# Kernel optimization log

Hardware: AMD Instinct MI355X
Metric: run time of the kernel (lower is better)

## Reference

```python
import jax, jax.numpy as jnp
import numpy as np

C = 128                      # channels per irrep
LS = [0, 0, 1, 1, 2, 2]      # active irreps (0e,0o,1e,1o,2e,2o), sorted order
D = C * sum(2 * l + 1 for l in LS)  # 2304
N = 100000                   # nodes


def setup_inputs() -> dict:
    key = jax.random.key(0)
    ks = jax.random.split(key, 7)
    inp = {"x": jax.random.normal(ks[0], (N, D), dtype=jnp.float32)}
    scale = 1.0 / np.sqrt(C)
    for name, k in zip(["W0p", "W0m", "W1p", "W1m", "W2p", "W2m"], ks[1:]):
        inp[name] = jax.random.normal(k, (C, C), dtype=jnp.float32) * scale
    return inp


def reference(x, W0p, W0m, W1p, W1m, W2p, W2m):
    # Split flat features into per-(l,parity) blocks [N, C, 2l+1],
    # mix channels per irrep (movedim + Linear in torch == einsum here),
    # merge back and add residual.
    Ws = [W0p, W0m, W1p, W1m, W2p, W2m]
    idx = 0
    parts = []
    for l, W in zip(LS, Ws):
        d = C * (2 * l + 1)
        blk = x[:, idx:idx + d].reshape(-1, C, 2 * l + 1)  # [N, C, m]
        idx += d
        y = jnp.einsum('ncm,dc->ndm', blk, W)              # channel mix per m
        parts.append(y.reshape(-1, d))
    return x + jnp.concatenate(parts, axis=-1)
```

## Files before the change

kernel.cpp:

```cpp
#include <hip/hip_runtime.h>
#include <hip/hip_bf16.h>

typedef float f32x4 __attribute__((ext_vector_type(4)));
typedef short s16x8 __attribute__((ext_vector_type(8)));

__device__ __forceinline__ unsigned short f32_to_bf16(float f){
    union { float f; unsigned u; } v; v.f = f;
    unsigned r = v.u + 0x7fffu + ((v.u >> 16) & 1u);
    return (unsigned short)(r >> 16);
}
__device__ __forceinline__ unsigned pack2(float a, float b){
    float2 t; t.x = a; t.y = b;
    __hip_bfloat162 h = __float22bfloat162_rn(t);
    union { __hip_bfloat162 h; unsigned u; } c; c.h = h;
    return c.u;
}

template<int N> __device__ __forceinline__ void wait_vmcnt(){
    if constexpr (N == 0)       asm volatile("s_waitcnt vmcnt(0)"  ::: "memory");
    else if constexpr (N == 3)  asm volatile("s_waitcnt vmcnt(3)"  ::: "memory");
    else if constexpr (N == 4)  asm volatile("s_waitcnt vmcnt(4)"  ::: "memory");
    else if constexpr (N == 5)  asm volatile("s_waitcnt vmcnt(5)"  ::: "memory");
    else if constexpr (N == 8)  asm volatile("s_waitcnt vmcnt(8)"  ::: "memory");
    else if constexpr (N == 9)  asm volatile("s_waitcnt vmcnt(9)"  ::: "memory");
    else if constexpr (N == 15) asm volatile("s_waitcnt vmcnt(15)" ::: "memory");
    else static_assert(N == 0, "add wait case");
    __builtin_amdgcn_sched_barrier(0);
}

__device__ __forceinline__ void bar_sync(){
    asm volatile("s_waitcnt lgkmcnt(0)" ::: "memory");
    __builtin_amdgcn_s_barrier();
    __builtin_amdgcn_sched_barrier(0);
}

__device__ __forceinline__ void dma16(const float* g, float* l){
    __builtin_amdgcn_global_load_lds(
        (const __attribute__((address_space(1))) unsigned int*)g,
        (__attribute__((address_space(3))) unsigned int*)l, 16, 0, 0);
}

__global__ __launch_bounds__(256)
void wconv_kernel(const float* __restrict__ W0p, const float* __restrict__ W0m,
                  const float* __restrict__ W1p, const float* __restrict__ W1m,
                  const float* __restrict__ W2p, const float* __restrict__ W2m,
                  unsigned short* __restrict__ wbf)
{
    const int idx = blockIdx.x * 256 + threadIdx.x;
    const int w  = idx >> 14;
    const int rc = idx & 16383;
    const float* Wp;
    switch (w) {
        case 0: Wp = W0p; break;  case 1: Wp = W0m; break;
        case 2: Wp = W1p; break;  case 3: Wp = W1m; break;
        case 4: Wp = W2p; break;  default: Wp = W2m; break;
    }
    const float v = Wp[rc] + (((rc >> 7) == (rc & 127)) ? 1.0f : 0.0f);
    wbf[idx] = f32_to_bf16(v);
}

template<int ML, int NT, int OCC>
__global__ __launch_bounds__(256, OCC)
void lx_dma(const float* __restrict__ x, const unsigned short* __restrict__ wbf,
            float* __restrict__ out, int yoff0, int yoff1, int w0, int ntiles)
{
    constexpr int BLK   = 128 * ML;
    constexpr int NTB   = NT * BLK;
    constexpr int DI    = NTB * 4 / 4096;
    constexpr int SI    = DI;
    constexpr int RROWS = NT * ML;
    constexpr int RTC   = (RROWS + 15) / 16;
    constexpr int PR    = RTC * 16;
    constexpr int LDSS  = 136;
    constexpr int CPT   = NTB / 256;
    constexpr int V4    = CPT / 4;

    __shared__ __attribute__((aligned(16))) float          lin[2][NTB];
    __shared__ __attribute__((aligned(16))) unsigned short lbf[PR * LDSS];
    __shared__ __attribute__((aligned(16))) float          lout[NTB];

    const int parity = blockIdx.y;
    const int yoff   = parity ? yoff1 : yoff0;
    const unsigned short* wb = wbf + (size_t)(w0 + parity) * 16384;

    const int tid = threadIdx.x;
    const int wv  = tid >> 6, ln = tid & 63;
    const int l16 = ln & 15,  lhi = ln >> 4;

    s16x8 bfr[4][2];
    #pragma unroll
    for (int s = 0; s < 4; ++s)
        #pragma unroll
        for (int tf = 0; tf < 2; ++tf)
            bfr[s][tf] = *reinterpret_cast<const s16x8*>(
                wb + (wv * 32 + tf * 16 + l16) * 128 + s * 32 + lhi * 8);

    const int pnl = tid >> 5;
    const int pc0 = (tid & 31) * 4;

    auto dma_tile = [&](int t, int cur) {
        const float* gb = x + (size_t)t * NT * 2304 + yoff;
        #pragma unroll
        for (int j = 0; j < DI; ++j) {
            const int chunk = j * 4 + wv;
            const int dw = chunk * 256 + ln * 4;
            const int nl = dw / BLK;
            const int r  = dw - nl * BLK;
            dma16(gb + (size_t)nl * 2304 + r, &lin[cur][chunk * 256]);
        }
    };
    auto flush_tile = [&](int t) {
        float* gb = out + (size_t)t * NT * 2304 + yoff;
        #pragma unroll
        for (int i = 0; i < SI; ++i) {
            const int dw = (i * 256 + tid) * 4;
            const int nl = dw / BLK;
            const int r  = dw - nl * BLK;
            *reinterpret_cast<float4*>(gb + (size_t)nl * 2304 + r) =
                *reinterpret_cast<const float4*>(&lout[dw]);
        }
    };

    const int G = (int)gridDim.x;
    int t = blockIdx.x, cur = 0;
    dma_tile(t, 0);
    if (t + G < ntiles) { dma_tile(t + G, 1); wait_vmcnt<DI>(); }
    else                { wait_vmcnt<0>(); }
    bar_sync();

    while (true) {
        {
            float v[CPT];
            const float* sp = &lin[cur][pnl * BLK + pc0 * ML];
            #pragma unroll
            for (int i = 0; i < V4; ++i) {
                const float4 t4 = *reinterpret_cast<const float4*>(sp + i * 4);
                v[i*4+0] = t4.x; v[i*4+1] = t4.y; v[i*4+2] = t4.z; v[i*4+3] = t4.w;
            }
            #pragma unroll
            for (int mm = 0; mm < ML; ++mm) {
                unsigned* wp = reinterpret_cast<unsigned*>(&lbf[(pnl * ML + mm) * LDSS + pc0]);
                wp[0] = pack2(v[mm],          v[ML + mm]);
                wp[1] = pack2(v[2*ML + mm],   v[3*ML + mm]);
            }
        }
        bar_sync();

        if (t + 2 * G < ntiles) dma_tile(t + 2 * G, cur);

        f32x4 acc[RTC][2];
        #pragma unroll
        for (int rt = 0; rt < RTC; ++rt) {
            acc[rt][0] = (f32x4){0.f,0.f,0.f,0.f};
            acc[rt][1] = (f32x4){0.f,0.f,0.f,0.f};
        }
        #pragma unroll
        for (int s = 0; s < 4; ++s) {
            const int k0 = s * 32 + lhi * 8;
            #pragma unroll
            for (int rt = 0; rt < RTC; ++rt) {
                const s16x8 af = *reinterpret_cast<const s16x8*>(
                    &lbf[(rt * 16 + l16) * LDSS + k0]);
                acc[rt][0] = __builtin_amdgcn_mfma_f32_16x16x32_bf16(af, bfr[s][0], acc[rt][0], 0, 0, 0);
                acc[rt][1] = __builtin_amdgcn_mfma_f32_16x16x32_bf16(af, bfr[s][1], acc[rt][1], 0, 0, 0);
            }
        }

        #pragma unroll
        for (int rt = 0; rt < RTC; ++rt)
            #pragma unroll
            for (int tf = 0; tf < 2; ++tf) {
                const int col = wv * 32 + tf * 16 + l16;
                #pragma unroll
                for (int j = 0; j < 4; ++j) {
                    const int row = rt * 16 + lhi * 4 + j;
                    if (row < RROWS) {
                        const int nl = row / ML;
                        lout[nl * BLK + col * ML + (row - nl * ML)] = acc[rt][tf][j];
                    }
                }
            }
        bar_sync();

        flush_tile(t);

        if (t + G >= ntiles) break;
        wait_vmcnt<2 * SI + DI>();
        bar_sync();
        t += G; cur ^= 1;
    }
}

template<int WGS>
__global__ __launch_bounds__(256, 4)
void l0_dma(const float* __restrict__ x, const unsigned short* __restrict__ wbf,
            float* __restrict__ out, int ntiles)
{
    constexpr int NT = 16;
    constexpr int DI = 4;
    constexpr int SI = 4;

    __shared__ __attribute__((aligned(16))) float lin[2][NT * 256];

    const int tid = threadIdx.x;
    const int wv  = tid >> 6, ln = tid & 63;
    const int l16 = ln & 15,  lhi = ln >> 4;
    const int b     = wv >> 1;
    const int dbase = (wv & 1) * 64;
    const unsigned short* wb = wbf + b * 16384;

    s16x8 afr[4][4];
    #pragma unroll
    for (int s = 0; s < 4; ++s)
        #pragma unroll
        for (int dt = 0; dt < 4; ++dt)
            afr[s][dt] = *reinterpret_cast<const s16x8*>(
                wb + (dbase + dt * 16 + l16) * 128 + s * 32 + lhi * 8);

    auto dma_tile = [&](int t, int cur) {
        const float* gb = x + (size_t)t * NT * 2304;
        float* lb = &lin[cur][0];
        #pragma unroll
        for (int j = 0; j < DI; ++j) {
            const int chunk = j * 4 + wv;
            const int dw   = chunk * 256 + ln * 4;
            const int node = dw >> 8;
            const int r    = dw & 255;
            dma16(gb + (size_t)node * 2304 + (r ^ ((node & 7) << 2)), lb + chunk * 256);
        }
    };

    const int tstart = blockIdx.x;
    int cur = 0;
    dma_tile(tstart, 0);
    if (tstart + WGS < ntiles) { dma_tile(tstart + WGS, 1); wait_vmcnt<4>(); }
    else                       { wait_vmcnt<0>(); }
    bar_sync();

    for (int t = tstart; t < ntiles; t += WGS, cur ^= 1) {
        const bool has1 = (t + WGS)     < ntiles;
        const bool has2 = (t + 2 * WGS) < ntiles;

        f32x4 acc[4];
        #pragma unroll
        for (int dt = 0; dt < 4; ++dt) acc[dt] = (f32x4){0.f,0.f,0.f,0.f};

        const float* bp = &lin[cur][0];
        const int nb = l16 * 256;
        const int sw = (l16 & 7) << 2;
        #pragma unroll
        for (int s = 0; s < 4; ++s) {
            const int c0 = b * 128 + s * 32 + lhi * 8;
            const float4 v0 = *reinterpret_cast<const float4*>(&bp[nb + ((c0    ) ^ sw)]);
            const float4 v1 = *reinterpret_cast<const float4*>(&bp[nb + ((c0 + 4) ^ sw)]);
            union { s16x8 v; unsigned u[4]; } bf;
            bf.u[0] = pack2(v0.x, v0.y); bf.u[1] = pack2(v0.z, v0.w);
            bf.u[2] = pack2(v1.x, v1.y); bf.u[3] = pack2(v1.z, v1.w);
            #pragma unroll
            for (int dt = 0; dt < 4; ++dt)
                acc[dt] = __builtin_amdgcn_mfma_f32_16x16x32_bf16(afr[s][dt], bf.v, acc[dt], 0, 0, 0);
        }

        bar_sync();

        float* dst = out + ((size_t)t * NT + l16) * 2304 + b * 128 + dbase + lhi * 4;
        #pragma unroll
        for (int dt = 0; dt < 4; ++dt) {
            float4 vv; vv.x = acc[dt][0]; vv.y = acc[dt][1];
                       vv.z = acc[dt][2]; vv.w = acc[dt][3];
            *reinterpret_cast<float4*>(dst + dt * 16) = vv;
        }

        if (has2) dma_tile(t + 2 * WGS, cur);
        if (has1) { if (has2) wait_vmcnt<8>(); else wait_vmcnt<4>(); }
        bar_sync();
    }
}

extern "C" void kernel_launch(void* const* d_in, const int* in_sizes, int n_in,
                              void* d_out, int out_size, void* d_ws, size_t ws_size,
                              hipStream_t stream) {
    const float* x   = (const float*)d_in[0];
    const float* W0p = (const float*)d_in[1];
    const float* W0m = (const float*)d_in[2];
    const float* W1p = (const float*)d_in[3];
    const float* W1m = (const float*)d_in[4];
    const float* W2p = (const float*)d_in[5];
    const float* W2m = (const float*)d_in[6];
    float* out = (float*)d_out;
    unsigned short* wbf = (unsigned short*)d_ws;

    const int N = in_sizes[0] / 2304;

    wconv_kernel<<<384, 256, 0, stream>>>(W0p, W0m, W1p, W1m, W2p, W2m, wbf);

    lx_dma<5, 8, 2><<<dim3(256, 2), 256, 0, stream>>>(x, wbf, out, 1024, 1664, 4, N / 8);
    lx_dma<3, 8, 3><<<dim3(384, 2), 256, 0, stream>>>(x, wbf, out, 256,  640,  2, N / 8);
    l0_dma<1024>   <<<1024,         256, 0, stream>>>(x, wbf, out, N / 16);
}
```

Measured before the change: 389.9 us.

## Fuse per-irrep kernels into one persistent launch with static block partition

Merges the three separate irrep kernels (l=2, l=1, l=0) into a single launch of 1024 blocks. Fixed block ranges are assigned to each irrep/parity using shared dynamic-style LDS. The l>0 path now uses tiles of 4 nodes instead of 8, with per-wave varying DMA counts and matching vmcnt waits. This aims to remove launch gaps and tail imbalance between back-to-back kernels so all streams run concurrently. The costs are a fixed work split that may not match bandwidth needs, smaller tiles with more per-tile overhead, and occupancy capped by the largest LDS footprint.

Measured after the change: 393.2 us. Within noise of the previous version (+0.8%).

```diff
diff --git a/kernel.cpp b/kernel.cpp
--- a/kernel.cpp
+++ b/kernel.cpp
@@ -18,14 +18,22 @@
 
 template<int N> __device__ __forceinline__ void wait_vmcnt(){
     if constexpr (N == 0)       asm volatile("s_waitcnt vmcnt(0)"  ::: "memory");
+    else if constexpr (N == 1)  asm volatile("s_waitcnt vmcnt(1)"  ::: "memory");
+    else if constexpr (N == 2)  asm volatile("s_waitcnt vmcnt(2)"  ::: "memory");
     else if constexpr (N == 3)  asm volatile("s_waitcnt vmcnt(3)"  ::: "memory");
     else if constexpr (N == 4)  asm volatile("s_waitcnt vmcnt(4)"  ::: "memory");
-    else if constexpr (N == 5)  asm volatile("s_waitcnt vmcnt(5)"  ::: "memory");
+    else if constexpr (N == 6)  asm volatile("s_waitcnt vmcnt(6)"  ::: "memory");
     else if constexpr (N == 8)  asm volatile("s_waitcnt vmcnt(8)"  ::: "memory");
     else if constexpr (N == 9)  asm volatile("s_waitcnt vmcnt(9)"  ::: "memory");
-    else if constexpr (N == 15) asm volatile("s_waitcnt vmcnt(15)" ::: "memory");
+    else if constexpr (N == 12) asm volatile("s_waitcnt vmcnt(12)" ::: "memory");
     else static_assert(N == 0, "add wait case");
     __builtin_amdgcn_sched_barrier(0);
+}
+
+template<int A, int B, int C, int D>
+__device__ __forceinline__ void wait_sel(bool first, bool has2){
+    if (first) { if (has2) wait_vmcnt<A>(); else wait_vmcnt<B>(); }
+    else       { if (has2) wait_vmcnt<C>(); else wait_vmcnt<D>(); }
 }
 
 __device__ __forceinline__ void bar_sync(){
@@ -59,29 +67,24 @@
     wbf[idx] = f32_to_bf16(v);
 }
 
-template<int ML, int NT, int OCC>
-__global__ __launch_bounds__(256, OCC)
-void lx_dma(const float* __restrict__ x, const unsigned short* __restrict__ wbf,
-            float* __restrict__ out, int yoff0, int yoff1, int w0, int ntiles)
+template<int ML>
+__device__ __forceinline__
+void lx_body(const float* __restrict__ x, const unsigned short* __restrict__ wb,
+             float* __restrict__ out, int yoff, int wg, int G, int ntiles,
+             char* smem)
 {
-    constexpr int BLK   = 128 * ML;
-    constexpr int NTB   = NT * BLK;
-    constexpr int DI    = NTB * 4 / 4096;
-    constexpr int SI    = DI;
-    constexpr int RROWS = NT * ML;
-    constexpr int RTC   = (RROWS + 15) / 16;
-    constexpr int PR    = RTC * 16;
-    constexpr int LDSS  = 136;
-    constexpr int CPT   = NTB / 256;
-    constexpr int V4    = CPT / 4;
-
-    __shared__ __attribute__((aligned(16))) float          lin[2][NTB];
-    __shared__ __attribute__((aligned(16))) unsigned short lbf[PR * LDSS];
-    __shared__ __attribute__((aligned(16))) float          lout[NTB];
-
-    const int parity = blockIdx.y;
-    const int yoff   = parity ? yoff1 : yoff0;
-    const unsigned short* wb = wbf + (size_t)(w0 + parity) * 16384;
+    constexpr int BLK  = 128 * ML;
+    constexpr int NTB  = 4 * BLK;
+    constexpr int CH   = NTB / 256;
+    constexpr int HI   = CH / 4 + 1;
+    constexpr int LO   = CH / 4;
+    constexpr int RROWS= 4 * ML;
+    constexpr int RTC  = (RROWS + 15) / 16;
+    constexpr int LDSS = 136;
+
+    float*          lin  = (float*)smem;
+    unsigned short* lbf  = (unsigned short*)(smem + 2*NTB*4);
+    float*          lout = (float*)(smem + 2*NTB*4 + RTC*16*LDSS*2);
 
     const int tid = threadIdx.x;
     const int wv  = tid >> 6, ln = tid & 63;
@@ -95,58 +98,54 @@
             bfr[s][tf] = *reinterpret_cast<const s16x8*>(
                 wb + (wv * 32 + tf * 16 + l16) * 128 + s * 32 + lhi * 8);
 
-    const int pnl = tid >> 5;
-    const int pc0 = (tid & 31) * 4;
-
     auto dma_tile = [&](int t, int cur) {
-        const float* gb = x + (size_t)t * NT * 2304 + yoff;
-        #pragma unroll
-        for (int j = 0; j < DI; ++j) {
-            const int chunk = j * 4 + wv;
-            const int dw = chunk * 256 + ln * 4;
-            const int nl = dw / BLK;
-            const int r  = dw - nl * BLK;
-            dma16(gb + (size_t)nl * 2304 + r, &lin[cur][chunk * 256]);
+        const float* gb = x + (size_t)t * 4 * 2304 + yoff;
+        float* lb = lin + cur * NTB;
+        #pragma unroll
+        for (int c = wv; c < CH; c += 4) {
+            const int dw = c * 256 + ln * 4;
+            const int nl = dw / BLK, r = dw - nl * BLK;
+            dma16(gb + (size_t)nl * 2304 + r, lb + c * 256);
         }
     };
     auto flush_tile = [&](int t) {
-        float* gb = out + (size_t)t * NT * 2304 + yoff;
-        #pragma unroll
-        for (int i = 0; i < SI; ++i) {
-            const int dw = (i * 256 + tid) * 4;
-            const int nl = dw / BLK;
-            const int r  = dw - nl * BLK;
+        float* gb = out + (size_t)t * 4 * 2304 + yoff;
+        #pragma unroll
+        for (int c = wv; c < CH; c += 4) {
+            const int dw = c * 256 + ln * 4;
+            const int nl = dw / BLK, r = dw - nl * BLK;
             *reinterpret_cast<float4*>(gb + (size_t)nl * 2304 + r) =
                 *reinterpret_cast<const float4*>(&lout[dw]);
         }
     };
 
-    const int G = (int)gridDim.x;
-    int t = blockIdx.x, cur = 0;
+    int t = wg, cur = 0;
+    bool has1 = (t + G) < ntiles;
     dma_tile(t, 0);
-    if (t + G < ntiles) { dma_tile(t + G, 1); wait_vmcnt<DI>(); }
-    else                { wait_vmcnt<0>(); }
+    if (has1) dma_tile(t + G, 1);
+    if (wv < 2) { if (has1) wait_vmcnt<HI>(); else wait_vmcnt<0>(); }
+    else        { if (has1) wait_vmcnt<LO>(); else wait_vmcnt<0>(); }
     bar_sync();
 
+    bool first = true;
     while (true) {
         {
-            float v[CPT];
-            const float* sp = &lin[cur][pnl * BLK + pc0 * ML];
-            #pragma unroll
-            for (int i = 0; i < V4; ++i) {
-                const float4 t4 = *reinterpret_cast<const float4*>(sp + i * 4);
-                v[i*4+0] = t4.x; v[i*4+1] = t4.y; v[i*4+2] = t4.z; v[i*4+3] = t4.w;
+            const float* sp = lin + cur * NTB + wv * BLK + ln * 2 * ML;
+            float v[2 * ML];
+            #pragma unroll
+            for (int i = 0; i < ML; ++i) {
+                const float2 t2 = *reinterpret_cast<const float2*>(sp + i * 2);
+                v[i * 2] = t2.x; v[i * 2 + 1] = t2.y;
             }
             #pragma unroll
-            for (int mm = 0; mm < ML; ++mm) {
-                unsigned* wp = reinterpret_cast<unsigned*>(&lbf[(pnl * ML + mm) * LDSS + pc0]);
-                wp[0] = pack2(v[mm],          v[ML + mm]);
-                wp[1] = pack2(v[2*ML + mm],   v[3*ML + mm]);
-            }
-        }
-        bar_sync();
-
-        if (t + 2 * G < ntiles) dma_tile(t + 2 * G, cur);
+            for (int mm = 0; mm < ML; ++mm)
+                *reinterpret_cast<unsigned*>(&lbf[(wv * ML + mm) * LDSS + ln * 2]) =
+                    pack2(v[mm], v[ML + mm]);
+        }
+        bar_sync();
+
+        const bool has2 = (t + 2 * G) < ntiles;
+        if (has2) dma_tile(t + 2 * G, cur);
 
         f32x4 acc[RTC][2];
         #pragma unroll
@@ -184,23 +183,20 @@
 
         flush_tile(t);
 
-        if (t + G >= ntiles) break;
-        wait_vmcnt<2 * SI + DI>();
-        bar_sync();
-        t += G; cur ^= 1;
+        has1 = (t + G) < ntiles;
+        if (!has1) break;
+        if (wv < 2) wait_sel<2*HI, HI, 3*HI, 2*HI>(first, has2);
+        else        wait_sel<2*LO, LO, 3*LO, 2*LO>(first, has2);
+        bar_sync();
+        t += G; cur ^= 1; first = false;
     }
 }
 
-template<int WGS>
-__global__ __launch_bounds__(256, 4)
-void l0_dma(const float* __restrict__ x, const unsigned short* __restrict__ wbf,
-            float* __restrict__ out, int ntiles)
+__device__ __forceinline__
+void l0_body(const float* __restrict__ x, const unsigned short* __restrict__ wbf,
+             float* __restrict__ out, int wg, int G, int ntiles, char* smem)
 {
-    constexpr int NT = 16;
-    constexpr int DI = 4;
-    constexpr int SI = 4;
-
-    __shared__ __attribute__((aligned(16))) float lin[2][NT * 256];
+    float* lin = (float*)smem;
 
     const int tid = threadIdx.x;
     const int wv  = tid >> 6, ln = tid & 63;
@@ -218,34 +214,30 @@
                 wb + (dbase + dt * 16 + l16) * 128 + s * 32 + lhi * 8);
 
     auto dma_tile = [&](int t, int cur) {
-        const float* gb = x + (size_t)t * NT * 2304;
-        float* lb = &lin[cur][0];
-        #pragma unroll
-        for (int j = 0; j < DI; ++j) {
-            const int chunk = j * 4 + wv;
-            const int dw   = chunk * 256 + ln * 4;
-            const int node = dw >> 8;
-            const int r    = dw & 255;
-            dma16(gb + (size_t)node * 2304 + (r ^ ((node & 7) << 2)), lb + chunk * 256);
+        const float* gb = x + (size_t)t * 16 * 2304;
+        float* lb = lin + cur * 4096;
+        #pragma unroll
+        for (int c = wv; c < 16; c += 4) {
+            const int dw = c * 256 + ln * 4;
+            const int node = dw >> 8, r = dw & 255;
+            dma16(gb + (size_t)node * 2304 + (r ^ ((node & 7) << 2)), lb + c * 256);
         }
     };
 
-    const int tstart = blockIdx.x;
-    int cur = 0;
-    dma_tile(tstart, 0);
-    if (tstart + WGS < ntiles) { dma_tile(tstart + WGS, 1); wait_vmcnt<4>(); }
-    else                       { wait_vmcnt<0>(); }
+    int t = wg, cur = 0;
+    bool has1 = (t + G) < ntiles;
+    dma_tile(t, 0);
+    if (has1) { dma_tile(t + G, 1); wait_vmcnt<4>(); } else wait_vmcnt<0>();
     bar_sync();
 
-    for (int t = tstart; t < ntiles; t += WGS, cur ^= 1) {
-        const bool has1 = (t + WGS)     < ntiles;
-        const bool has2 = (t + 2 * WGS) < ntiles;
+    while (true) {
+        const bool has2 = (t + 2 * G) < ntiles;
 
         f32x4 acc[4];
         #pragma unroll
         for (int dt = 0; dt < 4; ++dt) acc[dt] = (f32x4){0.f,0.f,0.f,0.f};
 
-        const float* bp = &lin[cur][0];
+        const float* bp = lin + cur * 4096;
         const int nb = l16 * 256;
         const int sw = (l16 & 7) << 2;
         #pragma unroll
@@ -260,10 +252,9 @@
             for (int dt = 0; dt < 4; ++dt)
                 acc[dt] = __builtin_amdgcn_mfma_f32_16x16x32_bf16(afr[s][dt], bf.v, acc[dt], 0, 0, 0);
         }
-
-        bar_sync();
-
-        float* dst = out + ((size_t)t * NT + l16) * 2304 + b * 128 + dbase + lhi * 4;
+        bar_sync();
+
+        float* dst = out + ((size_t)t * 16 + l16) * 2304 + b * 128 + dbase + lhi * 4;
         #pragma unroll
         for (int dt = 0; dt < 4; ++dt) {
             float4 vv; vv.x = acc[dt][0]; vv.y = acc[dt][1];
@@ -271,9 +262,33 @@
             *reinterpret_cast<float4*>(dst + dt * 16) = vv;
         }
 
-        if (has2) dma_tile(t + 2 * WGS, cur);
-        if (has1) { if (has2) wait_vmcnt<8>(); else wait_vmcnt<4>(); }
-        bar_sync();
+        if (has2) dma_tile(t + 2 * G, cur);
+        has1 = (t + G) < ntiles;
+        if (!has1) break;
+        if (has2) wait_vmcnt<8>(); else wait_vmcnt<4>();
+        bar_sync();
+        t += G; cur ^= 1;
+    }
+}
+
+#define SMEM_MAX 39424
+__global__ __launch_bounds__(256, 4)
+void fused_kernel(const float* __restrict__ x, const unsigned short* __restrict__ wbf,
+                  float* __restrict__ out, int n4, int n16)
+{
+    __shared__ __attribute__((aligned(16))) char smem[SMEM_MAX];
+    const int b = blockIdx.x;
+    if (b < 576) {
+        const int p = (b >= 288);
+        lx_body<5>(x, wbf + (size_t)(4 + p) * 16384, out,
+                   p ? 1664 : 1024, b - p * 288, 288, n4, smem);
+    } else if (b < 912) {
+        const int bb = b - 576;
+        const int p = (bb >= 168);
+        lx_body<3>(x, wbf + (size_t)(2 + p) * 16384, out,
+                   p ? 640 : 256, bb - p * 168, 168, n4, smem);
+    } else {
+        l0_body(x, wbf, out, b - 912, 112, n16, smem);
     }
 }
 
@@ -293,8 +308,5 @@
     const int N = in_sizes[0] / 2304;
 
     wconv_kernel<<<384, 256, 0, stream>>>(W0p, W0m, W1p, W1m, W2p, W2m, wbf);
-
-    lx_dma<5, 8, 2><<<dim3(256, 2), 256, 0, stream>>>(x, wbf, out, 1024, 1664, 4, N / 8);
-    lx_dma<3, 8, 3><<<dim3(384, 2), 256, 0, stream>>>(x, wbf, out, 256,  640,  2, N / 8);
-    l0_dma<1024>   <<<1024,         256, 0, stream>>>(x, wbf, out, N / 16);
-}
+    fused_kernel<<<1024, 256, 0, stream>>>(x, wbf, out, N / 4, N / 16);
+}
```
